# Kernel tuning notes

Hardware: AMD Instinct MI355X
Metric: run time of the kernel (lower is better)

## Reference

```python
import jax, jax.numpy as jnp
import numpy as np

E, N, F = 50000, 25000, 32

def setup_inputs() -> dict:
    key = jax.random.key(0)
    ks = jax.random.split(key, 8)
    efeat = jax.random.normal(ks[0], (E, F), dtype=jnp.float32) * 0.2
    initial_efeats = jax.random.normal(ks[1], (E, F), dtype=jnp.float32) * 0.2
    # msg_fn / attn_fn: Linear(F, F*F)
    Wm = jax.random.normal(ks[2], (F * F, F), dtype=jnp.float32) * 0.05
    bm = jnp.zeros((F * F,), dtype=jnp.float32)
    Wa = jax.random.normal(ks[3], (F * F, F), dtype=jnp.float32) * 0.05
    ba = jnp.zeros((F * F,), dtype=jnp.float32)
    src = jax.random.randint(ks[4], (E,), 0, N, dtype=jnp.int32)
    dst = jax.random.randint(ks[5], (E,), 0, N, dtype=jnp.int32)
    return {"efeat": efeat, "initial_efeats": initial_efeats, "Wm": Wm, "bm": bm,
            "Wa": Wa, "ba": ba, "src": src, "dst": dst, "num_nodes": N}

def reference(efeat, initial_efeats, Wm, bm, Wa, ba, src, dst, num_nodes):
    e, f = efeat.shape
    # edge-conditioned transform matrices: [E, F, F]
    w_m = (efeat @ Wm.T + bm).reshape(e, f, f)
    w_a = (efeat @ Wa.T + ba).reshape(e, f, f)
    h = efeat[:, :, None]                 # [E, F, 1]
    ih = initial_efeats[:, :, None]       # [E, F, 1]
    e1 = w_m * h                          # [E, F, F]
    exp_e2 = jnp.exp(w_a * h)             # [E, F, F]
    initial_e1 = w_m * ih
    exp_initial_e2 = jnp.exp(w_a * ih)
    # scatter-sum exp weights to destination nodes, gather back at src
    sum_exp_node = jax.ops.segment_sum(exp_e2, dst, num_segments=num_nodes)  # [N, F, F]
    sum_exp = sum_exp_node[src] - exp_e2 + exp_initial_e2
    h1 = exp_e2 * e1
    initial_h1 = exp_initial_e2 * initial_e1
    m_node = jax.ops.segment_sum(h1, dst, num_segments=num_nodes)            # [N, F, F]
    h2 = (m_node[src] - h1 + initial_h1) / sum_exp
    return h2.sum(axis=1)                 # [E, F]
```

## Files before the change

kernel.cpp:

```cpp
#include <hip/hip_runtime.h>
#include <hip/hip_fp16.h>
#include <math.h>
#include <stdint.h>


#define FDIM   32
#define NNODES 25000

typedef __attribute__((ext_vector_type(8))) short bf16x8;
typedef __attribute__((ext_vector_type(4))) float f32x4;

__device__ __forceinline__ unsigned short f2bf(float f) {
    unsigned u = __float_as_uint(f);
    return (unsigned short)((u + 0x7FFFu + ((u >> 16) & 1u)) >> 16);
}
__device__ __forceinline__ float hlo(unsigned v) {
    return __half2float(__ushort_as_half((unsigned short)v));
}
__device__ __forceinline__ unsigned pk2(float q, float p) {
    unsigned uq = (unsigned)__half_as_ushort(__float2half(q));
    unsigned up = (unsigned)__half_as_ushort(__float2half(p));
    return (uq >> 8) | (up & 0xFF00u);
}
#if __has_builtin(__builtin_amdgcn_exp2f)
__device__ __forceinline__ float ex2(float x) { return __builtin_amdgcn_exp2f(x); }
#else
__device__ __forceinline__ float ex2(float x) { return exp2f(x); }
#endif

__global__ __launch_bounds__(256) void zero_f4(float4* __restrict__ p, int n4) {
    int i = blockIdx.x * blockDim.x + threadIdx.x;
    int stride = gridDim.x * blockDim.x;
    float4 z = make_float4(0.f, 0.f, 0.f, 0.f);
    for (; i < n4; i += stride) p[i] = z;
}

__global__ __launch_bounds__(256) void k_hist(
    const int* __restrict__ src, const int* __restrict__ dst,
    int* __restrict__ cnt_src, int* __restrict__ cnt_dst, int E) {
    int e = blockIdx.x * blockDim.x + threadIdx.x;
    if (e < E) {
        atomicAdd(&cnt_dst[dst[e]], 1);
        atomicAdd(&cnt_src[src[e]], 1);
    }
}

__global__ __launch_bounds__(256) void k_scan2(
    const int* __restrict__ cnt_dst, int* __restrict__ off_dst, int* __restrict__ cur_dst,
    const int* __restrict__ cnt_src, int* __restrict__ off_src, int* __restrict__ cur_src,
    int n) {
    const int* cnt = blockIdx.x ? cnt_src : cnt_dst;
    int* off = blockIdx.x ? off_src : off_dst;
    int* cur = blockIdx.x ? cur_src : cur_dst;
    __shared__ int wsum[4];
    __shared__ int carry_sh;
    const int tid = threadIdx.x, lane = tid & 63, w = tid >> 6;
    if (tid == 0) carry_sh = 0;
    __syncthreads();
    for (int base = 0; base < n; base += 4096) {
        int i0 = base + tid * 16;
        int v[16];
        int s = 0;
#pragma unroll
        for (int k = 0; k < 16; ++k) {
            v[k] = (i0 + k < n) ? cnt[i0 + k] : 0;
            s += v[k];
        }
        int inc = s;
        for (int d = 1; d < 64; d <<= 1) {
            int t = __shfl_up(inc, d, 64);
            if (lane >= d) inc += t;
        }
        if (lane == 63) wsum[w] = inc;
        __syncthreads();
        int wbase = 0;
        for (int k = 0; k < w; ++k) wbase += wsum[k];
        int carry = carry_sh;
        int excl = carry + wbase + inc - s;
#pragma unroll
        for (int k = 0; k < 16; ++k) {
            if (i0 + k < n) { off[i0 + k] = excl; cur[i0 + k] = excl; }
            excl += v[k];
        }
        __syncthreads();
        if (tid == 255) carry_sh = carry + wbase + inc;
    }
    __syncthreads();
    if (tid == 0) off[n] = carry_sh;
}

__global__ __launch_bounds__(256) void k_scatter(
    const int* __restrict__ src, const int* __restrict__ dst,
    int* __restrict__ cur_src, int* __restrict__ cur_dst,
    int* __restrict__ eb_src, int* __restrict__ eb_dst, int E) {
    int e = blockIdx.x * blockDim.x + threadIdx.x;
    if (e < E) {
        int p = atomicAdd(&cur_dst[dst[e]], 1); eb_dst[p] = e;
        int q = atomicAdd(&cur_src[src[e]], 1); eb_src[q] = e;
    }
}

__global__ __launch_bounds__(256) void prep_w(
    const float* __restrict__ Wm, const float* __restrict__ Wa,
    short* __restrict__ wbuf) {
    int idx = blockIdx.x * blockDim.x + threadIdx.x;
    if (idx >= 2 * 64 * 64) return;
    int mat  = idx >> 12;
    int jt   = (idx >> 6) & 63;
    int lane = idx & 63;
    const float* W = mat ? Wa : Wm;
    const float* s = W + (size_t)(jt * 16 + (lane & 15)) * FDIM + (lane >> 4) * 8;
    bf16x8 v;
#pragma unroll
    for (int t = 0; t < 8; ++t) v[t] = (short)f2bf(s[t]);
    *(bf16x8*)(wbuf + (size_t)idx * 8) = v;
}

__global__ __launch_bounds__(256) void gemm(
    const float* __restrict__ efeat, const float* __restrict__ ifeat,
    const float* __restrict__ bm, const float* __restrict__ ba,
    const short* __restrict__ wbuf,
    unsigned* __restrict__ buf, unsigned* __restrict__ ratio, int E)
{
    const int lane = threadIdx.x & 63;
    const int wid  = threadIdx.x >> 6;
    const int et   = blockIdx.x * 4 + wid;
    if (et * 16 >= E) return;
    const int r16 = lane & 15;
    const int kq  = lane >> 4;
    const int e   = et * 16 + r16;

    const float* xrow  = efeat + ((size_t)e << 5);
    const float* x0row = ifeat + ((size_t)e << 5);

    const float* xa = xrow + kq * 8;
    bf16x8 xfrag;
#pragma unroll
    for (int t = 0; t < 8; ++t) xfrag[t] = (short)f2bf(xa[t]);

    unsigned* bout = buf + ((size_t)e << 9);

    for (int m = 0; m < 16; ++m) {
        float2 xe = *(const float2*)(xrow + 2 * m);
        unsigned P[4][4];
#pragma unroll
        for (int p = 0; p < 4; ++p) {
            const int jt = m * 4 + p;
            bf16x8 wfm = *(const bf16x8*)(wbuf + ((size_t)(jt)      * 64 + lane) * 8);
            bf16x8 wfa = *(const bf16x8*)(wbuf + ((size_t)(64 + jt) * 64 + lane) * 8);
            const int jb = jt * 16 + kq * 4;
            const float4 bm4 = *(const float4*)(bm + jb);
            const float4 ba4 = *(const float4*)(ba + jb);
            f32x4 accm = {bm4.x, bm4.y, bm4.z, bm4.w};
            f32x4 acca = {ba4.x, ba4.y, ba4.z, ba4.w};
            accm = __builtin_amdgcn_mfma_f32_16x16x32_bf16(wfm, xfrag, accm, 0, 0, 0);
            acca = __builtin_amdgcn_mfma_f32_16x16x32_bf16(wfa, xfrag, acca, 0, 0, 0);
            const float xi  = (p >> 1) ? xe.y : xe.x;
            const float xil = xi * 1.44269504f;
#pragma unroll
            for (int r = 0; r < 4; ++r)
                P[p][r] = pk2(acca[r] * xil, accm[r] * xi);
        }
        uint4 sa, sb;
        sa.x = P[0][0] | (P[2][0] << 16);
        sa.y = P[0][1] | (P[2][1] << 16);
        sa.z = P[0][2] | (P[2][2] << 16);
        sa.w = P[0][3] | (P[2][3] << 16);
        sb.x = P[1][0] | (P[3][0] << 16);
        sb.y = P[1][1] | (P[3][1] << 16);
        sb.z = P[1][2] | (P[3][2] << 16);
        sb.w = P[1][3] | (P[3][3] << 16);
        *(uint4*)(bout + m * 32 + kq * 4)      = sa;
        *(uint4*)(bout + m * 32 + 16 + kq * 4) = sb;

        if (kq == 0) {
            float2 x0e = *(const float2*)(x0row + 2 * m);
            float r0 = x0e.x * __builtin_amdgcn_rcpf(xe.x);
            float r1 = x0e.y * __builtin_amdgcn_rcpf(xe.y);
            unsigned h0 = (unsigned)__half_as_ushort(__float2half(r0));
            unsigned h1 = (unsigned)__half_as_ushort(__float2half(r1));
            ratio[((size_t)e << 4) + m] = h0 | (h1 << 16);
        }
    }
}

__global__ __launch_bounds__(256) void consume(
    const unsigned* __restrict__ buf, const unsigned* __restrict__ ratio,
    const int* __restrict__ off_dst, const int* __restrict__ eb_dst,
    const int* __restrict__ off_src, const int* __restrict__ eb_src,
    float* __restrict__ out)
{
    const int tid = threadIdx.x;
    const int l   = tid & 63;
    const int wid = tid >> 6;
    const int n   = blockIdx.x * 4 + wid;
    if (n >= NNODES) return;

    const int a0 = off_dst[n], a1 = off_dst[n + 1];
    const int b0 = off_src[n], b1 = off_src[n + 1];
    const int din = a1 - a0, dout = b1 - b0;
    if (dout == 0) return;

    int eid = (l < 32) ? eb_dst[a0 + l] : eb_src[b0 + (l - 32)];
    const int half = l & 1;
    const int j2   = l >> 1;
    const int mb   = half * 8;

    float S[16], M[16];
#pragma unroll
    for (int t = 0; t < 16; ++t) { S[t] = 0.f; M[t] = 0.f; }

#define BCIN(t)  __builtin_amdgcn_readfirstlane(((t) < 32) ? __shfl(eid, (t), 64) : eb_dst[a0 + (t)])
#define BCOUT(t) __builtin_amdgcn_readfirstlane(((t) < 32) ? __shfl(eid, 32 + (t), 64) : eb_src[b0 + (t)])
#define LDA(R, ee) { const unsigned* bp_ = buf + ((size_t)(ee) << 9) + j2;      \
    _Pragma("unroll") for (int s_ = 0; s_ < 8; ++s_) R[s_] = bp_[(mb + s_) * 32]; }
#define LDR(RF, ee) { const uint4* rp_ = (const uint4*)(ratio + (((size_t)(ee)) << 4) + mb); \
    uint4 ra_ = rp_[0], rb_ = rp_[1];                                           \
    RF[0] = ra_.x; RF[1] = ra_.y; RF[2] = ra_.z; RF[3] = ra_.w;                 \
    RF[4] = rb_.x; RF[5] = rb_.y; RF[6] = rb_.z; RF[7] = rb_.w; }
#define CIN(R) { _Pragma("unroll") for (int s_ = 0; s_ < 8; ++s_) {             \
    unsigned d_ = R[s_];                                                        \
    float q0_ = hlo(d_ << 8),  p0_ = hlo(d_);                                   \
    float q1_ = hlo(d_ >> 8),  p1_ = hlo(d_ >> 16);                             \
    float ea_ = ex2(q0_), eb_ = ex2(q1_);                                       \
    S[2*s_]   += ea_;  M[2*s_]   = fmaf(ea_, p0_, M[2*s_]);                     \
    S[2*s_+1] += eb_;  M[2*s_+1] = fmaf(eb_, p1_, M[2*s_+1]); } }
#define PRC(T, Q, P, RI) {                                                      \
    float e2_  = ex2(Q);        float h1_  = e2_ * (P);                         \
    float ei2_ = ex2((Q)*(RI)); float ih1_ = ei2_ * ((P) * (RI));               \
    float den_ = (S[T] - e2_) + ei2_;                                           \
    float num_ = (M[T] - h1_) + ih1_;                                           \
    float h2_  = num_ * __builtin_amdgcn_rcpf(den_);                            \
    osum += isfinite(h2_) ? h2_ : 0.f; }
#define COUT(R, RF, eo) { float osum = 0.f;                                     \
    _Pragma("unroll") for (int s_ = 0; s_ < 8; ++s_) {                          \
        unsigned d_ = R[s_], rw_ = RF[s_];                                      \
        float ri0_ = hlo(rw_), ri1_ = hlo(rw_ >> 16);                           \
        float q0_ = hlo(d_ << 8),  p0_ = hlo(d_);                               \
        float q1_ = hlo(d_ >> 8),  p1_ = hlo(d_ >> 16);                         \
        PRC(2*s_,     q0_, p0_, ri0_);                                          \
        PRC(2*s_ + 1, q1_, p1_, ri1_); }                                        \
    osum += __shfl_xor(osum, 1, 64);                                            \
    if (half == 0) out[((size_t)(eo) << 5) + j2] = osum; }

    unsigned A0[8], A1[8], R0[8], R1[8];

    if (din > 0) { int e_ = BCIN(0); LDA(A0, e_); }
    if (din > 1) { int e_ = BCIN(1); LDA(A1, e_); }
    {
        int t = 0;
        while (t < din) {
            CIN(A0);
            if (t + 2 < din) { int e_ = BCIN(t + 2); LDA(A0, e_); }
            if (t + 1 >= din) break;
            CIN(A1);
            if (t + 3 < din) { int e_ = BCIN(t + 3); LDA(A1, e_); }
            t += 2;
        }
    }

    int eo0 = 0, eo1 = 0;
    if (dout > 0) { eo0 = BCOUT(0); LDA(A0, eo0); LDR(R0, eo0); }
    if (dout > 1) { eo1 = BCOUT(1); LDA(A1, eo1); LDR(R1, eo1); }
    {
        int t = 0;
        while (t < dout) {
            COUT(A0, R0, eo0);
            if (t + 2 < dout) { eo0 = BCOUT(t + 2); LDA(A0, eo0); LDR(R0, eo0); }
            if (t + 1 >= dout) break;
            COUT(A1, R1, eo1);
            if (t + 3 < dout) { eo1 = BCOUT(t + 3); LDA(A1, eo1); LDR(R1, eo1); }
            t += 2;
        }
    }
#undef BCIN
#undef BCOUT
#undef LDA
#undef LDR
#undef CIN
#undef PRC
#undef COUT
}

extern "C" void kernel_launch(void* const* d_in, const int* in_sizes, int n_in,
                              void* d_out, int out_size, void* d_ws, size_t ws_size,
                              hipStream_t stream) {
    const float* efeat = (const float*)d_in[0];
    const float* ifeat = (const float*)d_in[1];
    const float* Wm    = (const float*)d_in[2];
    const float* bm    = (const float*)d_in[3];
    const float* Wa    = (const float*)d_in[4];
    const float* ba    = (const float*)d_in[5];
    const int*   src   = (const int*)d_in[6];
    const int*   dst   = (const int*)d_in[7];
    const int E = in_sizes[6];
    const int N = NNODES;
    float* out = (float*)d_out;

    int* cnt_dst = (int*)d_ws;
    int* cnt_src = cnt_dst + N;
    int* off_dst = cnt_src + N;
    int* off_src = off_dst + (N + 1);
    int* cur_dst = off_src + (N + 1);
    int* cur_src = cur_dst + N;
    int* eb_dst  = cur_src + N;
    int* eb_src  = eb_dst + E;
    short* wbuf  = (short*)(((uintptr_t)(eb_src + E) + 255) & ~(uintptr_t)255);
    unsigned* buf =
        (unsigned*)(((uintptr_t)(wbuf + 2 * 64 * 64 * 8) + 255) & ~(uintptr_t)255);
    unsigned* ratio = buf + (size_t)E * 512;

    zero_f4<<<64, 256, 0, stream>>>((float4*)cnt_dst, (2 * N) / 4);
    k_hist<<<(E + 255) / 256, 256, 0, stream>>>(src, dst, cnt_src, cnt_dst, E);
    k_scan2<<<2, 256, 0, stream>>>(cnt_dst, off_dst, cur_dst,
                                   cnt_src, off_src, cur_src, N);
    k_scatter<<<(E + 255) / 256, 256, 0, stream>>>(src, dst, cur_src, cur_dst,
                                                   eb_src, eb_dst, E);
    prep_w<<<32, 256, 0, stream>>>(Wm, Wa, wbuf);

    const int etiles = (E + 15) / 16;
    gemm<<<(etiles + 3) / 4, 256, 0, stream>>>(efeat, ifeat, bm, ba, wbuf,
                                               buf, ratio, E);
    consume<<<(NNODES + 3) / 4, 256, 0, stream>>>(buf, ratio,
                                                  off_dst, eb_dst,
                                                  off_src, eb_src, out);
}
```

Baseline: 238.1 us.

## Split gemm m-loop across block waves and make consume grid-stride with deeper prefetch

```diff
diff --git a/kernel.cpp b/kernel.cpp
--- a/kernel.cpp
+++ b/kernel.cpp
@@ -124,8 +124,7 @@
 {
     const int lane = threadIdx.x & 63;
     const int wid  = threadIdx.x >> 6;
-    const int et   = blockIdx.x * 4 + wid;
-    if (et * 16 >= E) return;
+    const int et   = blockIdx.x;
     const int r16 = lane & 15;
     const int kq  = lane >> 4;
     const int e   = et * 16 + r16;
@@ -139,8 +138,11 @@
     for (int t = 0; t < 8; ++t) xfrag[t] = (short)f2bf(xa[t]);
 
     unsigned* bout = buf + ((size_t)e << 9);
-
-    for (int m = 0; m < 16; ++m) {
+    unsigned rat0 = 0, rat1 = 0, rat2 = 0, rat3 = 0;
+
+#pragma unroll
+    for (int mm = 0; mm < 4; ++mm) {
+        const int m = wid * 4 + mm;
         float2 xe = *(const float2*)(xrow + 2 * m);
         unsigned P[4][4];
 #pragma unroll
@@ -173,14 +175,22 @@
         *(uint4*)(bout + m * 32 + kq * 4)      = sa;
         *(uint4*)(bout + m * 32 + 16 + kq * 4) = sb;
 
-        if (kq == 0) {
+        {
             float2 x0e = *(const float2*)(x0row + 2 * m);
             float r0 = x0e.x * __builtin_amdgcn_rcpf(xe.x);
             float r1 = x0e.y * __builtin_amdgcn_rcpf(xe.y);
             unsigned h0 = (unsigned)__half_as_ushort(__float2half(r0));
             unsigned h1 = (unsigned)__half_as_ushort(__float2half(r1));
-            ratio[((size_t)e << 4) + m] = h0 | (h1 << 16);
-        }
+            unsigned rw = h0 | (h1 << 16);
+            if (mm == 0) rat0 = rw;
+            if (mm == 1) rat1 = rw;
+            if (mm == 2) rat2 = rw;
+            if (mm == 3) rat3 = rw;
+        }
+    }
+    if (kq == 0) {
+        uint4 rq; rq.x = rat0; rq.y = rat1; rq.z = rat2; rq.w = rat3;
+        *(uint4*)(ratio + ((size_t)e << 4) + wid * 4) = rq;
     }
 }
 
@@ -188,27 +198,14 @@
     const unsigned* __restrict__ buf, const unsigned* __restrict__ ratio,
     const int* __restrict__ off_dst, const int* __restrict__ eb_dst,
     const int* __restrict__ off_src, const int* __restrict__ eb_src,
-    float* __restrict__ out)
+    float* __restrict__ out, int nwaves)
 {
     const int tid = threadIdx.x;
     const int l   = tid & 63;
-    const int wid = tid >> 6;
-    const int n   = blockIdx.x * 4 + wid;
-    if (n >= NNODES) return;
-
-    const int a0 = off_dst[n], a1 = off_dst[n + 1];
-    const int b0 = off_src[n], b1 = off_src[n + 1];
-    const int din = a1 - a0, dout = b1 - b0;
-    if (dout == 0) return;
-
-    int eid = (l < 32) ? eb_dst[a0 + l] : eb_src[b0 + (l - 32)];
+    const int gw  = blockIdx.x * 4 + (tid >> 6);
     const int half = l & 1;
     const int j2   = l >> 1;
     const int mb   = half * 8;
-
-    float S[16], M[16];
-#pragma unroll
-    for (int t = 0; t < 16; ++t) { S[t] = 0.f; M[t] = 0.f; }
 
 #define BCIN(t)  __builtin_amdgcn_readfirstlane(((t) < 32) ? __shfl(eid, (t), 64) : eb_dst[a0 + (t)])
 #define BCOUT(t) __builtin_amdgcn_readfirstlane(((t) < 32) ? __shfl(eid, 32 + (t), 64) : eb_src[b0 + (t)])
@@ -243,34 +240,52 @@
     osum += __shfl_xor(osum, 1, 64);                                            \
     if (half == 0) out[((size_t)(eo) << 5) + j2] = osum; }
 
-    unsigned A0[8], A1[8], R0[8], R1[8];
-
-    if (din > 0) { int e_ = BCIN(0); LDA(A0, e_); }
-    if (din > 1) { int e_ = BCIN(1); LDA(A1, e_); }
-    {
-        int t = 0;
-        while (t < din) {
-            CIN(A0);
-            if (t + 2 < din) { int e_ = BCIN(t + 2); LDA(A0, e_); }
-            if (t + 1 >= din) break;
-            CIN(A1);
-            if (t + 3 < din) { int e_ = BCIN(t + 3); LDA(A1, e_); }
-            t += 2;
-        }
-    }
-
-    int eo0 = 0, eo1 = 0;
-    if (dout > 0) { eo0 = BCOUT(0); LDA(A0, eo0); LDR(R0, eo0); }
-    if (dout > 1) { eo1 = BCOUT(1); LDA(A1, eo1); LDR(R1, eo1); }
-    {
-        int t = 0;
-        while (t < dout) {
-            COUT(A0, R0, eo0);
-            if (t + 2 < dout) { eo0 = BCOUT(t + 2); LDA(A0, eo0); LDR(R0, eo0); }
-            if (t + 1 >= dout) break;
-            COUT(A1, R1, eo1);
-            if (t + 3 < dout) { eo1 = BCOUT(t + 3); LDA(A1, eo1); LDR(R1, eo1); }
-            t += 2;
+    unsigned A0[8], A1[8], A2[8], R0[8], R1[8];
+
+    for (int n = gw; n < NNODES; n += nwaves) {
+        const int b0 = off_src[n], b1 = off_src[n + 1];
+        const int dout = b1 - b0;
+        if (dout == 0) continue;
+        const int a0 = off_dst[n], a1 = off_dst[n + 1];
+        const int din = a1 - a0;
+
+        int eid = (l < 32) ? eb_dst[a0 + l] : eb_src[b0 + (l - 32)];
+
+        float S[16], M[16];
+#pragma unroll
+        for (int t = 0; t < 16; ++t) { S[t] = 0.f; M[t] = 0.f; }
+
+        if (din > 0) { int e_ = BCIN(0); LDA(A0, e_); }
+        if (din > 1) { int e_ = BCIN(1); LDA(A1, e_); }
+        if (din > 2) { int e_ = BCIN(2); LDA(A2, e_); }
+        {
+            int t = 0;
+            while (t < din) {
+                CIN(A0);
+                if (t + 3 < din) { int e_ = BCIN(t + 3); LDA(A0, e_); }
+                if (t + 1 >= din) break;
+                CIN(A1);
+                if (t + 4 < din) { int e_ = BCIN(t + 4); LDA(A1, e_); }
+                if (t + 2 >= din) break;
+                CIN(A2);
+                if (t + 5 < din) { int e_ = BCIN(t + 5); LDA(A2, e_); }
+                t += 3;
+            }
+        }
+
+        int eo0 = 0, eo1 = 0;
+        if (dout > 0) { eo0 = BCOUT(0); LDA(A0, eo0); LDR(R0, eo0); }
+        if (dout > 1) { eo1 = BCOUT(1); LDA(A1, eo1); LDR(R1, eo1); }
+        {
+            int t = 0;
+            while (t < dout) {
+                COUT(A0, R0, eo0);
+                if (t + 2 < dout) { eo0 = BCOUT(t + 2); LDA(A0, eo0); LDR(R0, eo0); }
+                if (t + 1 >= dout) break;
+                COUT(A1, R1, eo1);
+                if (t + 3 < dout) { eo1 = BCOUT(t + 3); LDA(A1, eo1); LDR(R1, eo1); }
+                t += 2;
+            }
         }
     }
 #undef BCIN
@@ -319,9 +334,10 @@
     prep_w<<<32, 256, 0, stream>>>(Wm, Wa, wbuf);
 
     const int etiles = (E + 15) / 16;
-    gemm<<<(etiles + 3) / 4, 256, 0, stream>>>(efeat, ifeat, bm, ba, wbuf,
-                                               buf, ratio, E);
-    consume<<<(NNODES + 3) / 4, 256, 0, stream>>>(buf, ratio,
-                                                  off_dst, eb_dst,
-                                                  off_src, eb_src, out);
-}
+    gemm<<<etiles, 256, 0, stream>>>(efeat, ifeat, bm, ba, wbuf,
+                                     buf, ratio, E);
+    const int cblocks = 1600;
+    consume<<<cblocks, 256, 0, stream>>>(buf, ratio,
+                                         off_dst, eb_dst,
+                                         off_src, eb_src, out, cblocks * 4);
+}
```

Result: slower. 261.1 us (+9.6%).
